# Kernel tuning notes

Hardware: AMD Instinct MI355X
Metric: run time of the kernel (lower is better)

## Reference

```python
import jax, jax.numpy as jnp
import numpy as np
from jax import lax

B, DIM, H, W = 8, 256, 48, 48
HEADS, DH = 8, 32
K, S = 5, 2
P = K // 2
SCALE = DH ** -0.5
EPS = 1e-5


def setup_inputs() -> dict:
    key = jax.random.key(0)
    ks = jax.random.split(key, 12)
    w = lambda k, sh: jax.random.normal(k, sh, jnp.float32) * 0.02
    return {
        'x': jax.random.normal(ks[0], (B, DIM, H, W), jnp.float32),
        'kv': jax.random.normal(ks[1], (B, DIM, H, W), jnp.float32),
        'wq': w(ks[2], (DIM, DIM)), 'bq': jnp.zeros((DIM,), jnp.float32),
        'wk': w(ks[3], (DIM, DIM)), 'bk': jnp.zeros((DIM,), jnp.float32),
        'wv': w(ks[4], (DIM, DIM)), 'bv': jnp.zeros((DIM,), jnp.float32),
        'w_dw': w(ks[5], (DH, 1, K, K)), 'b_dw': jnp.zeros((DH,), jnp.float32),
        'ln_w': jnp.ones((DH,), jnp.float32), 'ln_b': jnp.zeros((DH,), jnp.float32),
        'w_off': w(ks[6], (2, DH)),
        'wo': w(ks[7], (DIM, DIM)), 'bo': jnp.zeros((DIM,), jnp.float32),
    }


def conv1x1(x, w, b=None):
    # x: (B, Cin, H, W), w: (Cout, Cin)
    y = jnp.einsum('oc,bchw->bohw', w, x)
    return y if b is None else y + b[None, :, None, None]


def grid_sample_bilinear(inp, grid):
    # inp: (N, C, Hh, Ww); grid: (N, Hg, Wg, 2) in (x, y), align_corners=True
    N, C, Hh, Ww = inp.shape
    gx = (grid[..., 0] + 1.0) * 0.5 * (Ww - 1)
    gy = (grid[..., 1] + 1.0) * 0.5 * (Hh - 1)
    x0 = jnp.floor(gx)
    y0 = jnp.floor(gy)
    wx = gx - x0  # frac weights for x1/y1 corners
    wy = gy - y0
    x0i = jnp.clip(x0.astype(jnp.int32), 0, Ww - 1)
    x1i = jnp.clip(x0.astype(jnp.int32) + 1, 0, Ww - 1)
    y0i = jnp.clip(y0.astype(jnp.int32), 0, Hh - 1)
    y1i = jnp.clip(y0.astype(jnp.int32) + 1, 0, Hh - 1)
    flat = inp.reshape(N, C, Hh * Ww)
    n = grid.shape[1] * grid.shape[2]

    def gather(yi, xi):
        idx = (yi * Ww + xi).reshape(N, 1, n)
        return jnp.take_along_axis(flat, jnp.broadcast_to(idx, (N, C, n)), axis=2)

    w00 = ((1 - wx) * (1 - wy)).reshape(N, 1, n)
    w01 = (wx * (1 - wy)).reshape(N, 1, n)
    w10 = ((1 - wx) * wy).reshape(N, 1, n)
    w11 = (wx * wy).reshape(N, 1, n)
    return (w00 * gather(y0i, x0i) + w01 * gather(y0i, x1i)
            + w10 * gather(y1i, x0i) + w11 * gather(y1i, x1i))  # (N, C, n)


def reference(x, kv, wq, bq, wk, bk, wv, bv, w_dw, b_dw, ln_w, ln_b, w_off, wo, bo):
    q = conv1x1(x, wq, bq)                      # (B, DIM, H, W)
    q_off = q.reshape(B * HEADS, DH, H, W)      # per-head channels
    # depthwise offset conv
    t = lax.conv_general_dilated(q_off, w_dw, (S, S), [(P, P), (P, P)],
                                 feature_group_count=DH,
                                 dimension_numbers=('NCHW', 'OIHW', 'NCHW'))
    t = t + b_dw[None, :, None, None]
    Hk, Wk = t.shape[2], t.shape[3]
    n = Hk * Wk
    # LayerNormProxy: LN over channel dim
    t = t.transpose(0, 2, 3, 1)                 # (BH, Hk, Wk, DH)
    mu = t.mean(-1, keepdims=True)
    var = ((t - mu) ** 2).mean(-1, keepdims=True)
    t = (t - mu) / jnp.sqrt(var + EPS) * ln_w + ln_b
    t = jax.nn.gelu(t, approximate=False)
    offset = jnp.einsum('oc,bhwc->bhwo', w_off, t)  # (BH, Hk, Wk, 2) as (y, x)
    # reference points, normalized to [-1, 1]
    ref_y = (jnp.linspace(0.5, Hk - 0.5, Hk, dtype=jnp.float32) / (Hk - 1.0)) * 2.0 - 1.0
    ref_x = (jnp.linspace(0.5, Wk - 0.5, Wk, dtype=jnp.float32) / (Wk - 1.0)) * 2.0 - 1.0
    ref = jnp.stack(jnp.meshgrid(ref_y, ref_x, indexing='ij'), axis=-1)  # (Hk, Wk, 2)
    pos = jnp.clip(offset + ref[None], -1.0, 1.0)
    grid = pos[..., ::-1]                       # (x, y) order for sampling
    kvs = grid_sample_bilinear(kv.reshape(B * HEADS, DH, H, W), grid)  # (BH, DH, n)
    kv4 = kvs.reshape(B, DIM, 1, n)
    k = conv1x1(kv4, wk, bk).reshape(B * HEADS, DH, n)
    v = conv1x1(kv4, wv, bv).reshape(B * HEADS, DH, n)
    qf = q.reshape(B * HEADS, DH, H * W)
    attn = jax.nn.softmax(jnp.einsum('bcm,bcn->bmn', qf, k) * SCALE, axis=2)
    out = jnp.einsum('bmn,bcn->bcm', attn, v).reshape(B, DIM, H, W)
    return conv1x1(out, wo, bo)
```

## Files before the change

### kernel.cpp

```cpp
#include <hip/hip_runtime.h>
#include <hip/hip_bf16.h>
#include <cstddef>

#define BB 8
#define DIM 256
#define HH 48
#define WW 48
#define HW 2304
#define HEADS 8
#define DH 32
#define BH 64
#define HK 24
#define WK 24
#define NN 576
#define SCALE 0.17677669529663687f
#define EPSF 1e-5f

typedef __attribute__((ext_vector_type(8))) short short8;
typedef __attribute__((ext_vector_type(4))) float f32x4;

static __device__ inline short f2bf_s(float f) {
  __hip_bfloat16 h = __float2bfloat16(f);
  return *reinterpret_cast<short*>(&h);
}

static __device__ inline unsigned pkrnd(float a, float b) {
  unsigned ua = __builtin_bit_cast(unsigned, a) + 0x8000u;
  unsigned ub = __builtin_bit_cast(unsigned, b) + 0x8000u;
  return __builtin_amdgcn_perm(ub, ua, 0x07060302);
}

static __device__ inline void split8(const float* xf, short8& bh, short8& bl) {
  union { unsigned u[4]; short8 v; } H, L;
#pragma unroll
  for (int p = 0; p < 4; p++) {
    float x0 = xf[2 * p], x1 = xf[2 * p + 1];
    unsigned u0 = __builtin_bit_cast(unsigned, x0) & 0xffff0000u;
    unsigned u1 = __builtin_bit_cast(unsigned, x1) & 0xffff0000u;
    float l0 = x0 - __builtin_bit_cast(float, u0);
    float l1 = x1 - __builtin_bit_cast(float, u1);
    H.u[p] = __builtin_amdgcn_perm(u1, u0, 0x07060302);
    L.u[p] = __builtin_amdgcn_perm(__builtin_bit_cast(unsigned, l1),
                                   __builtin_bit_cast(unsigned, l0), 0x07060302);
  }
  bh = H.v;
  bl = L.v;
}

__global__ __launch_bounds__(256) void prep(
    const float* __restrict__ x, const float* __restrict__ kv,
    const float* __restrict__ wq, const float* __restrict__ wk,
    const float* __restrict__ wv, const float* __restrict__ wo,
    short* __restrict__ Xh, short* __restrict__ Xl,
    float* __restrict__ kvT,
    short* __restrict__ Wqh, short* __restrict__ Wql,
    short* __restrict__ Wkh, short* __restrict__ Wkl,
    short* __restrict__ Wvh, short* __restrict__ Wvl,
    short* __restrict__ Woh, short* __restrict__ Wol) {
  __shared__ float t[64][65];
  const int bid = blockIdx.x;
  if (bid < 1152) {
    int mt = bid % 36, t2 = bid / 36;
    int ct = t2 & 3, b = t2 >> 2;
    const int c0 = ct * 64, m0 = mt * 64;
    const int col = threadIdx.x & 63, row4 = threadIdx.x >> 6;
    const float* xb = x + ((size_t)b * 256 + c0) * HW + m0;
#pragma unroll
    for (int k = 0; k < 16; k++) {
      int c = row4 + k * 4;
      t[c][col] = xb[(size_t)c * HW + col];
    }
    __syncthreads();
    short* oh = Xh + ((size_t)b * HW + m0) * 256 + c0;
    short* ol = Xl + ((size_t)b * HW + m0) * 256 + c0;
#pragma unroll
    for (int k = 0; k < 16; k++) {
      int m = row4 + k * 4;
      float v = t[col][m];
      unsigned u = __builtin_bit_cast(unsigned, v) & 0xffff0000u;
      float rem = v - __builtin_bit_cast(float, u);
      oh[(size_t)m * 256 + col] = (short)(u >> 16);
      ol[(size_t)m * 256 + col] = (short)(__builtin_bit_cast(unsigned, rem) >> 16);
    }
  } else if (bid < 2304) {
    int bb = bid - 1152;
    int mt = bb % 36, t2 = bb / 36;
    int ct = t2 & 3, b = t2 >> 2;
    const int c0 = ct * 64, m0 = mt * 64;
    const int col = threadIdx.x & 63, row4 = threadIdx.x >> 6;
    const float* xb = kv + ((size_t)b * 256 + c0) * HW + m0;
#pragma unroll
    for (int k = 0; k < 16; k++) {
      int c = row4 + k * 4;
      t[c][col] = xb[(size_t)c * HW + col];
    }
    __syncthreads();
    float* ot = kvT + ((size_t)b * HW + m0) * 256 + c0;
#pragma unroll
    for (int k = 0; k < 16; k++) {
      int m = row4 + k * 4;
      ot[(size_t)m * 256 + col] = t[col][m];
    }
  } else {
    const float* srcs[4] = {wq, wk, wv, wo};
    short* his[4] = {Wqh, Wkh, Wvh, Woh};
    short* los[4] = {Wql, Wkl, Wvl, Wol};
    int e0 = (bid - 2304) * 1024 + threadIdx.x * 4;
    int w = e0 >> 16, off = e0 & 65535;
    float4 v4 = *(const float4*)(srcs[w] + off);
    float vv[4] = {v4.x, v4.y, v4.z, v4.w};
    union { short s[4]; int2 i2; } Hu, Lu;
#pragma unroll
    for (int j = 0; j < 4; j++) {
      unsigned u = __builtin_bit_cast(unsigned, vv[j]) & 0xffff0000u;
      float rem = vv[j] - __builtin_bit_cast(float, u);
      Hu.s[j] = (short)(u >> 16);
      Lu.s[j] = (short)(__builtin_bit_cast(unsigned, rem) >> 16);
    }
    *(int2*)(his[w] + off) = Hu.i2;
    *(int2*)(los[w] + off) = Lu.i2;
  }
}

__global__ __launch_bounds__(256) void gemm_q_mfma(const short* __restrict__ Wh,
                                                   const short* __restrict__ Wl,
                                                   const float* __restrict__ bias,
                                                   const short* __restrict__ Xh,
                                                   const short* __restrict__ Xl,
                                                   float* __restrict__ Y) {
  const int tid = threadIdx.x;
  const int wave = tid >> 6;
  const int lane = tid & 63;
  const int quad = lane >> 4, l15 = lane & 15;
  const int b = blockIdx.y;
  const int oBase = wave * 64;
  const int mBase = blockIdx.x * 64;

  f32x4 acc[4][4] = {};
  for (int kc = 0; kc < 256; kc += 32) {
    short8 ah[4], al[4];
#pragma unroll
    for (int os = 0; os < 4; os++) {
      ah[os] = *(const short8*)(Wh + (size_t)(oBase + os * 16 + l15) * 256 + kc + quad * 8);
      al[os] = *(const short8*)(Wl + (size_t)(oBase + os * 16 + l15) * 256 + kc + quad * 8);
    }
#pragma unroll
    for (int mt = 0; mt < 4; mt++) {
      short8 bh_ = *(const short8*)(Xh + ((size_t)b * HW + mBase + mt * 16 + l15) * 256 + kc + quad * 8);
      short8 bl_ = *(const short8*)(Xl + ((size_t)b * HW + mBase + mt * 16 + l15) * 256 + kc + quad * 8);
#pragma unroll
      for (int os = 0; os < 4; os++) {
        acc[os][mt] = __builtin_amdgcn_mfma_f32_16x16x32_bf16(ah[os], bh_, acc[os][mt], 0, 0, 0);
        acc[os][mt] = __builtin_amdgcn_mfma_f32_16x16x32_bf16(al[os], bh_, acc[os][mt], 0, 0, 0);
        acc[os][mt] = __builtin_amdgcn_mfma_f32_16x16x32_bf16(ah[os], bl_, acc[os][mt], 0, 0, 0);
      }
    }
  }

#pragma unroll
  for (int os = 0; os < 4; os++)
#pragma unroll
    for (int r = 0; r < 4; r++) {
      int o = oBase + os * 16 + quad * 4 + r;
      float bs = bias[o];
      float* yp = Y + ((size_t)b * 256 + o) * HW + mBase + l15;
#pragma unroll
      for (int mt = 0; mt < 4; mt++) yp[mt * 16] = acc[os][mt][r] + bs;
    }
}

#define QPS 101
__global__ __launch_bounds__(256) void dw_sample_kernel(
    const float* __restrict__ q, const float* __restrict__ kvT,
    const float* __restrict__ w_dw, const float* __restrict__ b_dw,
    const float* __restrict__ ln_w, const float* __restrict__ ln_b,
    const float* __restrict__ w_off, short* __restrict__ kvsTh,
    short* __restrict__ kvsTl) {
  __shared__ float s_q[32 * QPS];
  __shared__ float s_w[DH * 25];
  const int tid = threadIdx.x;
  const int ch = tid & 31;
  const int np = tid >> 5;
  const int bid = blockIdx.x;
  const int b = bid & 7;
  const int r = bid >> 3;
  const int head = r / 72;
  const int rr = r - head * 72;
  const int yk = rr / 3;
  const int xk0 = (rr - yk * 3) * 8;
  const int bh = b * 8 + head;
  const int xk = xk0 + np;
  const int n = yk * WK + xk;

  for (int i = tid; i < DH * 25; i += 256) s_w[i] = w_dw[i];

  {
    const int y0 = yk * 2 - 2, x0 = xk0 * 2 - 2;
    const float* qbh = q + (size_t)bh * DH * HW;
#pragma unroll
    for (int it = 0; it < 13; it++) {
      int e = it * 256 + tid;
      if (e < 3200) {
        int c = e / 100;
        int rem = e - c * 100;
        int dy = rem / 20;
        int xl = rem - dy * 20;
        int gy = y0 + dy, gx = x0 + xl;
        float v = 0.f;
        if ((unsigned)gy < HH && (unsigned)gx < WW)
          v = qbh[(size_t)c * HW + gy * WW + gx];
        s_q[c * QPS + dy * 20 + xl] = v;
      }
    }
  }
  __syncthreads();

  float t = b_dw[ch];
  {
    const float* wp = s_w + ch * 25;
    const float* qp = s_q + ch * QPS + np * 2;
#pragma unroll
    for (int dy = 0; dy < 5; dy++)
#pragma unroll
      for (int dx = 0; dx < 5; dx++)
        t += wp[dy * 5 + dx] * qp[dy * 20 + dx];
  }

  float mu = t;
#pragma unroll
  for (int m = 1; m < 32; m <<= 1) mu += __shfl_xor(mu, m);
  mu *= (1.0f / DH);
  float d = t - mu;
  float var = d * d;
#pragma unroll
  for (int m = 1; m < 32; m <<= 1) var += __shfl_xor(var, m);
  var *= (1.0f / DH);
  float rstd = rsqrtf(var + EPSF);

  float xn = d * rstd * ln_w[ch] + ln_b[ch];
  float g = 0.5f * xn * (1.0f + erff(xn * 0.70710678118654752f));
  float o0 = w_off[ch] * g;
  float o1 = w_off[DH + ch] * g;
#pragma unroll
  for (int m = 1; m < 32; m <<= 1) {
    o0 += __shfl_xor(o0, m);
    o1 += __shfl_xor(o1, m);
  }

  const float ref_y = (0.5f + (float)yk) / 23.0f * 2.0f - 1.0f;
  const float ref_x = (0.5f + (float)xk) / 23.0f * 2.0f - 1.0f;
  float py = fminf(fmaxf(o0 + ref_y, -1.0f), 1.0f);
  float px = fminf(fmaxf(o1 + ref_x, -1.0f), 1.0f);

  float gx = (px + 1.0f) * 0.5f * 47.0f;
  float gy = (py + 1.0f) * 0.5f * 47.0f;
  float x0f = floorf(gx), y0f = floorf(gy);
  float wx = gx - x0f, wy = gy - y0f;
  int x0 = (int)x0f, y0 = (int)y0f;
  int x0i = min(max(x0, 0), WW - 1);
  int x1i = min(max(x0 + 1, 0), WW - 1);
  int y0i = min(max(y0, 0), HH - 1);
  int y1i = min(max(y0 + 1, 0), HH - 1);
  float w00 = (1.f - wx) * (1.f - wy);
  float w01 = wx * (1.f - wy);
  float w10 = (1.f - wx) * wy;
  float w11 = wx * wy;

  const float* kvb = kvT + (size_t)b * HW * 256 + head * DH + ch;
  float val = w00 * kvb[(size_t)(y0i * WW + x0i) * 256]
            + w01 * kvb[(size_t)(y0i * WW + x1i) * 256]
            + w10 * kvb[(size_t)(y1i * WW + x0i) * 256]
            + w11 * kvb[(size_t)(y1i * WW + x1i) * 256];

  unsigned ub = __builtin_bit_cast(unsigned, val);
  unsigned uh = ub & 0xffff0000u;
  float rem = val - __builtin_bit_cast(float, uh);
  size_t idx = ((size_t)b * NN + n) * 256 + head * DH + ch;
  kvsTh[idx] = (short)(uh >> 16);
  kvsTl[idx] = (short)(__builtin_bit_cast(unsigned, rem) >> 16);
}

__global__ __launch_bounds__(256) void kv_gemm_mfma(
    const short* __restrict__ Wkh, const short* __restrict__ Wkl,
    const float* __restrict__ bk,
    const short* __restrict__ Wvh, const short* __restrict__ Wvl,
    const float* __restrict__ bv,
    const short* __restrict__ Xh, const short* __restrict__ Xl,
    short* __restrict__ Kb, short* __restrict__ Vb) {
  const int tid = threadIdx.x;
  const int wave = tid >> 6;
  const int lane = tid & 63;
  const int quad = lane >> 4, l15 = lane & 15;
  const int b = blockIdx.z;
  const int mode = blockIdx.y >> 2;
  const int oTile = (blockIdx.y & 3) * 64;
  const int nBase = blockIdx.x * 64;

  if (mode == 0) {
    const int nW = nBase + wave * 16;
    const short* arh = Xh + ((size_t)b * NN + nW + l15) * 256 + quad * 8;
    const short* arl = Xl + ((size_t)b * NN + nW + l15) * 256 + quad * 8;
    f32x4 acc[4] = {};
    for (int kc = 0; kc < 256; kc += 32) {
      short8 ah = *(const short8*)(arh + kc);
      short8 al = *(const short8*)(arl + kc);
#pragma unroll
      for (int ot = 0; ot < 4; ot++) {
        short8 bh_ = *(const short8*)(Wkh + (size_t)(oTile + ot * 16 + l15) * 256 + kc + quad * 8);
        short8 bl_ = *(const short8*)(Wkl + (size_t)(oTile + ot * 16 + l15) * 256 + kc + quad * 8);
        acc[ot] = __builtin_amdgcn_mfma_f32_16x16x32_bf16(ah, bh_, acc[ot], 0, 0, 0);
        acc[ot] = __builtin_amdgcn_mfma_f32_16x16x32_bf16(al, bh_, acc[ot], 0, 0, 0);
        acc[ot] = __builtin_amdgcn_mfma_f32_16x16x32_bf16(ah, bl_, acc[ot], 0, 0, 0);
      }
    }
    float bs[4];
#pragma unroll
    for (int ot = 0; ot < 4; ot++) bs[ot] = bk[oTile + ot * 16 + l15];
#pragma unroll
    for (int r = 0; r < 4; r++) {
      short* yp = Kb + ((size_t)b * NN + nW + quad * 4 + r) * 256 + oTile + l15;
#pragma unroll
      for (int ot = 0; ot < 4; ot++) yp[ot * 16] = f2bf_s(acc[ot][r] + bs[ot]);
    }
  } else {
    const int oW = oTile + wave * 16;
    const short* arh = Wvh + (size_t)(oW + l15) * 256 + quad * 8;
    const short* arl = Wvl + (size_t)(oW + l15) * 256 + quad * 8;
    f32x4 acc[4] = {};
    for (int kc = 0; kc < 256; kc += 32) {
      short8 ah = *(const short8*)(arh + kc);
      short8 al = *(const short8*)(arl + kc);
#pragma unroll
      for (int nt = 0; nt < 4; nt++) {
        short8 bh_ = *(const short8*)(Xh + ((size_t)b * NN + nBase + nt * 16 + l15) * 256 + kc + quad * 8);
        short8 bl_ = *(const short8*)(Xl + ((size_t)b * NN + nBase + nt * 16 + l15) * 256 + kc + quad * 8);
        acc[nt] = __builtin_amdgcn_mfma_f32_16x16x32_bf16(ah, bh_, acc[nt], 0, 0, 0);
        acc[nt] = __builtin_amdgcn_mfma_f32_16x16x32_bf16(al, bh_, acc[nt], 0, 0, 0);
        acc[nt] = __builtin_amdgcn_mfma_f32_16x16x32_bf16(ah, bl_, acc[nt], 0, 0, 0);
      }
    }
#pragma unroll
    for (int r = 0; r < 4; r++) {
      int o = oW + quad * 4 + r;
      float bs = bv[o];
      short* yp = Vb + ((size_t)b * 256 + o) * NN + nBase + l15;
#pragma unroll
      for (int nt = 0; nt < 4; nt++) yp[nt * 16] = f2bf_s(acc[nt][r] + bs);
    }
  }
}

__global__ __launch_bounds__(256) void attn_mfma(const float* __restrict__ q,
                                                 const short* __restrict__ Kb,
                                                 const short* __restrict__ Vb,
                                                 short* __restrict__ O) {
  __shared__ short sK[2][64 * 40];
  __shared__ short sV[2][32 * 88];
  __shared__ int sP[4][2][256];
  const int tid = threadIdx.x;
  const int wave = tid >> 6;
  const int lane = tid & 63;
  const int quad = lane >> 4;
  const int l15 = lane & 15;
  const int bh = blockIdx.y;
  const int b = bh >> 3, head = bh & 7;
  const int mBase = blockIdx.x * 128 + wave * 32;

  short8 bq[2];
#pragma unroll
  for (int mt = 0; mt < 2; mt++) {
    const float* qp = q + ((size_t)bh * DH + quad * 8) * HW + mBase + mt * 16 + l15;
    short8 v;
#pragma unroll
    for (int j = 0; j < 8; j++) v[j] = f2bf_s(qp[(size_t)j * HW] * SCALE);
    bq[mt] = v;
  }

  const int kn = tid >> 2, kc = (tid & 3) * 8;
  const int vc = tid >> 3, vn = (tid & 7) * 8;
  const short* kg = Kb + (size_t)b * NN * 256 + head * DH;
  const short* vg = Vb + ((size_t)b * 256 + head * DH) * NN;

  short8 kreg = *(const short8*)(kg + (size_t)kn * 256 + kc);
  short8 vreg = *(const short8*)(vg + (size_t)vc * NN + vn);
  *(short8*)(&sK[0][kn * 40 + kc]) = kreg;
  *(short8*)(&sV[0][vc * 88 + vn]) = vreg;
  __syncthreads();

  const int g = (l15 >> 1) & 3;
  const int row16 = l15 * 16;
  const int wr0 = row16 + (((quad >> 1) ^ g) << 2) + ((quad & 1) << 1);
  const int wr1 = row16 + (((2 + (quad >> 1)) ^ g) << 2) + ((quad & 1) << 1);
  const int rd = row16 + ((quad ^ g) << 2);

  f32x4 oacc[2][2] = {};
  f32x4 dacc[2] = {};
  const short ONE = 0x3F80;
  const short8 ones = {ONE, ONE, ONE, ONE, ONE, ONE, ONE, ONE};

  for (int s = 0; s < 9; s++) {
    const int buf = s & 1;
    if (s + 1 < 9) {
      kreg = *(const short8*)(kg + (size_t)((s + 1) * 64 + kn) * 256 + kc);
      vreg = *(const short8*)(vg + (size_t)vc * NN + (s + 1) * 64 + vn);
    }
#pragma unroll
    for (int nt = 0; nt < 2; nt++) {
      short8 ka0 = *(const short8*)(&sK[buf][(nt * 32 + l15) * 40 + quad * 8]);
      short8 ka1 = *(const short8*)(&sK[buf][(nt * 32 + 16 + l15) * 40 + quad * 8]);
      short8 va0 = *(const short8*)(&sV[buf][l15 * 88 + nt * 32 + quad * 8]);
      short8 va1 = *(const short8*)(&sV[buf][(16 + l15) * 88 + nt * 32 + quad * 8]);
      f32x4 z = {0.f, 0.f, 0.f, 0.f};
      f32x4 st[2][2];
      st[0][0] = __builtin_amdgcn_mfma_f32_16x16x32_bf16(ka0, bq[0], z, 0, 0, 0);
      st[0][1] = __builtin_amdgcn_mfma_f32_16x16x32_bf16(ka1, bq[0], z, 0, 0, 0);
      st[1][0] = __builtin_amdgcn_mfma_f32_16x16x32_bf16(ka0, bq[1], z, 0, 0, 0);
      st[1][1] = __builtin_amdgcn_mfma_f32_16x16x32_bf16(ka1, bq[1], z, 0, 0, 0);
#pragma unroll
      for (int mt = 0; mt < 2; mt++) {
        float p0 = __expf(st[mt][0][0]), p1 = __expf(st[mt][0][1]);
        float p2 = __expf(st[mt][0][2]), p3 = __expf(st[mt][0][3]);
        float p4 = __expf(st[mt][1][0]), p5 = __expf(st[mt][1][1]);
        float p6 = __expf(st[mt][1][2]), p7 = __expf(st[mt][1][3]);
        int* base = &sP[wave][mt][0];
        *(int2*)(base + wr0) = make_int2((int)pkrnd(p0, p1), (int)pkrnd(p2, p3));
        *(int2*)(base + wr1) = make_int2((int)pkrnd(p4, p5), (int)pkrnd(p6, p7));
      }
#pragma unroll
      for (int mt = 0; mt < 2; mt++) {
        short8 pa = *(short8*)(&sP[wave][mt][0] + rd);
        oacc[mt][0] = __builtin_amdgcn_mfma_f32_16x16x32_bf16(pa, va0, oacc[mt][0], 0, 0, 0);
        oacc[mt][1] = __builtin_amdgcn_mfma_f32_16x16x32_bf16(pa, va1, oacc[mt][1], 0, 0, 0);
        dacc[mt] = __builtin_amdgcn_mfma_f32_16x16x32_bf16(pa, ones, dacc[mt], 0, 0, 0);
      }
    }
    if (s + 1 < 9) {
      *(short8*)(&sK[buf ^ 1][kn * 40 + kc]) = kreg;
      *(short8*)(&sV[buf ^ 1][vc * 88 + vn]) = vreg;
    }
    __syncthreads();
  }

#pragma unroll
  for (int mt = 0; mt < 2; mt++) {
    short* ob = O + ((size_t)b * HW + mBase + mt * 16) * 256 + head * DH + l15;
#pragma unroll
    for (int r = 0; r < 4; r++) {
      float inv = 1.0f / dacc[mt][r];
      ob[(size_t)(quad * 4 + r) * 256] = f2bf_s(oacc[mt][0][r] * inv);
      ob[(size_t)(quad * 4 + r) * 256 + 16] = f2bf_s(oacc[mt][1][r] * inv);
    }
  }
}

__global__ __launch_bounds__(256) void wo_gemm_mfma(const short* __restrict__ Whi,
                                                    const short* __restrict__ Wlo,
                                                    const float* __restrict__ bias,
                                                    const short* __restrict__ X,
                                                    float* __restrict__ Y) {
  const int tid = threadIdx.x;
  const int wave = tid >> 6;
  const int lane = tid & 63;
  const int quad = lane >> 4;
  const int l15 = lane & 15;
  const int b = blockIdx.y;
  const int oBase = wave * 64;
  const int mBase = blockIdx.x * 64;

  f32x4 acc[4][4] = {};
  for (int kc = 0; kc < 256; kc += 32) {
    short8 ah[4], al[4];
#pragma unroll
    for (int os = 0; os < 4; os++) {
      ah[os] = *(const short8*)(Whi + (size_t)(oBase + os * 16 + l15) * 256 + kc + quad * 8);
      al[os] = *(const short8*)(Wlo + (size_t)(oBase + os * 16 + l15) * 256 + kc + quad * 8);
    }
#pragma unroll
    for (int mt = 0; mt < 4; mt++) {
      short8 bx = *(const short8*)(X + ((size_t)b * HW + mBase + mt * 16 + l15) * 256 + kc + quad * 8);
#pragma unroll
      for (int os = 0; os < 4; os++) {
        acc[os][mt] = __builtin_amdgcn_mfma_f32_16x16x32_bf16(ah[os], bx, acc[os][mt], 0, 0, 0);
        acc[os][mt] = __builtin_amdgcn_mfma_f32_16x16x32_bf16(al[os], bx, acc[os][mt], 0, 0, 0);
      }
    }
  }

#pragma unroll
  for (int os = 0; os < 4; os++)
#pragma unroll
    for (int r = 0; r < 4; r++) {
      int o = oBase + os * 16 + quad * 4 + r;
      float bs = bias[o];
      float* yp = Y + ((size_t)b * 256 + o) * HW + mBase + l15;
#pragma unroll
      for (int mt = 0; mt < 4; mt++) yp[mt * 16] = acc[os][mt][r] + bs;
    }
}

extern "C" void kernel_launch(void* const* d_in, const int* in_sizes, int n_in,
                              void* d_out, int out_size, void* d_ws, size_t ws_size,
                              hipStream_t stream) {
  const float* x    = (const float*)d_in[0];
  const float* kv   = (const float*)d_in[1];
  const float* wq   = (const float*)d_in[2];
  const float* bq   = (const float*)d_in[3];
  const float* wk   = (const float*)d_in[4];
  const float* bk   = (const float*)d_in[5];
  const float* wv   = (const float*)d_in[6];
  const float* bv   = (const float*)d_in[7];
  const float* w_dw = (const float*)d_in[8];
  const float* b_dw = (const float*)d_in[9];
  const float* ln_w = (const float*)d_in[10];
  const float* ln_b = (const float*)d_in[11];
  const float* w_off= (const float*)d_in[12];
  const float* wo   = (const float*)d_in[13];
  const float* bo   = (const float*)d_in[14];
  float* out = (float*)d_out;
  float* ws = (float*)d_ws;

  float* q     = ws;
  short* Xth   = (short*)(ws + 4718592);
  short* O     = (short*)(ws + 4718592);
  short* Xtl   = (short*)(ws + 7077888);
  short* kvsTh = (short*)(ws + 7077888);
  short* kvsTl = (short*)(ws + 7667712);
  short* Kb    = (short*)(ws + 8257536);
  short* Vb    = (short*)(ws + 8847360);
  short* Wqh   = (short*)(ws + 9437184);
  short* Wql = Wqh + 65536;
  short* Wkh = Wql + 65536;
  short* Wkl = Wkh + 65536;
  short* Wvh = Wkl + 65536;
  short* Wvl = Wvh + 65536;
  short* Woh = Wvl + 65536;
  short* Wol = Woh + 65536;
  float* kvT = out;

  prep<<<dim3(2560), dim3(256), 0, stream>>>(x, kv, wq, wk, wv, wo, Xth, Xtl, kvT,
                                             Wqh, Wql, Wkh, Wkl, Wvh, Wvl, Woh, Wol);
  gemm_q_mfma<<<dim3(HW / 64, BB), dim3(256), 0, stream>>>(Wqh, Wql, bq, Xth, Xtl, q);
  dw_sample_kernel<<<dim3(BH * NN / 8), dim3(256), 0, stream>>>(
      q, kvT, w_dw, b_dw, ln_w, ln_b, w_off, kvsTh, kvsTl);
  kv_gemm_mfma<<<dim3(NN / 64, 8, BB), dim3(256), 0, stream>>>(
      Wkh, Wkl, bk, Wvh, Wvl, bv, kvsTh, kvsTl, Kb, Vb);
  attn_mfma<<<dim3(HW / 128, BH), dim3(256), 0, stream>>>(q, Kb, Vb, O);
  wo_gemm_mfma<<<dim3(HW / 64, BB), dim3(256), 0, stream>>>(Woh, Wol, bo, O, out);
}
```

Before: 254.5 us.

## Co-schedule kv transpose and weight splits with Q GEMM; stage activations in LDS

Moves the kv transpose and the wk/wv/wo hi/lo split out of the prep kernel and into the Q-projection GEMM launch as extra block ranges, so that independent work overlaps with the GEMM. The Q and Wo GEMMs now use 512-thread blocks that stage the 64-row activation tile into XOR-swizzled shared memory and split the output channels across 8 waves instead of 4. The aim is to cut redundant global loads of the activation tile and raise parallelism per block. In exchange, each block uses 64KB of LDS in the fused GEMM, which may limit occupancy.

```diff
diff --git a/kernel.cpp b/kernel.cpp
--- a/kernel.cpp
+++ b/kernel.cpp
@@ -30,33 +30,10 @@
   return __builtin_amdgcn_perm(ub, ua, 0x07060302);
 }
 
-static __device__ inline void split8(const float* xf, short8& bh, short8& bl) {
-  union { unsigned u[4]; short8 v; } H, L;
-#pragma unroll
-  for (int p = 0; p < 4; p++) {
-    float x0 = xf[2 * p], x1 = xf[2 * p + 1];
-    unsigned u0 = __builtin_bit_cast(unsigned, x0) & 0xffff0000u;
-    unsigned u1 = __builtin_bit_cast(unsigned, x1) & 0xffff0000u;
-    float l0 = x0 - __builtin_bit_cast(float, u0);
-    float l1 = x1 - __builtin_bit_cast(float, u1);
-    H.u[p] = __builtin_amdgcn_perm(u1, u0, 0x07060302);
-    L.u[p] = __builtin_amdgcn_perm(__builtin_bit_cast(unsigned, l1),
-                                   __builtin_bit_cast(unsigned, l0), 0x07060302);
-  }
-  bh = H.v;
-  bl = L.v;
-}
-
 __global__ __launch_bounds__(256) void prep(
-    const float* __restrict__ x, const float* __restrict__ kv,
-    const float* __restrict__ wq, const float* __restrict__ wk,
-    const float* __restrict__ wv, const float* __restrict__ wo,
+    const float* __restrict__ x, const float* __restrict__ wq,
     short* __restrict__ Xh, short* __restrict__ Xl,
-    float* __restrict__ kvT,
-    short* __restrict__ Wqh, short* __restrict__ Wql,
-    short* __restrict__ Wkh, short* __restrict__ Wkl,
-    short* __restrict__ Wvh, short* __restrict__ Wvl,
-    short* __restrict__ Woh, short* __restrict__ Wol) {
+    short* __restrict__ Wqh, short* __restrict__ Wql) {
   __shared__ float t[64][65];
   const int bid = blockIdx.x;
   if (bid < 1152) {
@@ -82,32 +59,9 @@
       oh[(size_t)m * 256 + col] = (short)(u >> 16);
       ol[(size_t)m * 256 + col] = (short)(__builtin_bit_cast(unsigned, rem) >> 16);
     }
-  } else if (bid < 2304) {
-    int bb = bid - 1152;
-    int mt = bb % 36, t2 = bb / 36;
-    int ct = t2 & 3, b = t2 >> 2;
-    const int c0 = ct * 64, m0 = mt * 64;
-    const int col = threadIdx.x & 63, row4 = threadIdx.x >> 6;
-    const float* xb = kv + ((size_t)b * 256 + c0) * HW + m0;
-#pragma unroll
-    for (int k = 0; k < 16; k++) {
-      int c = row4 + k * 4;
-      t[c][col] = xb[(size_t)c * HW + col];
-    }
-    __syncthreads();
-    float* ot = kvT + ((size_t)b * HW + m0) * 256 + c0;
-#pragma unroll
-    for (int k = 0; k < 16; k++) {
-      int m = row4 + k * 4;
-      ot[(size_t)m * 256 + col] = t[col][m];
-    }
   } else {
-    const float* srcs[4] = {wq, wk, wv, wo};
-    short* his[4] = {Wqh, Wkh, Wvh, Woh};
-    short* los[4] = {Wql, Wkl, Wvl, Wol};
-    int e0 = (bid - 2304) * 1024 + threadIdx.x * 4;
-    int w = e0 >> 16, off = e0 & 65535;
-    float4 v4 = *(const float4*)(srcs[w] + off);
+    int e0 = (bid - 1152) * 1024 + threadIdx.x * 4;
+    float4 v4 = *(const float4*)(wq + e0);
     float vv[4] = {v4.x, v4.y, v4.z, v4.w};
     union { short s[4]; int2 i2; } Hu, Lu;
 #pragma unroll
@@ -117,56 +71,116 @@
       Hu.s[j] = (short)(u >> 16);
       Lu.s[j] = (short)(__builtin_bit_cast(unsigned, rem) >> 16);
     }
+    *(int2*)(Wqh + e0) = Hu.i2;
+    *(int2*)(Wql + e0) = Lu.i2;
+  }
+}
+
+__global__ __launch_bounds__(512) void gemm_q_fused(
+    const short* __restrict__ Wh, const short* __restrict__ Wl,
+    const float* __restrict__ bias,
+    const short* __restrict__ Xh, const short* __restrict__ Xl,
+    float* __restrict__ Y,
+    const float* __restrict__ kv, float* __restrict__ kvT,
+    const float* __restrict__ wk, const float* __restrict__ wv,
+    const float* __restrict__ wo,
+    short* __restrict__ Wkh, short* __restrict__ Wkl,
+    short* __restrict__ Wvh, short* __restrict__ Wvl,
+    short* __restrict__ Woh, short* __restrict__ Wol) {
+  __shared__ short sB[2][64 * 256];
+  const int bid = blockIdx.x;
+  const int tid = threadIdx.x;
+
+  if (bid < 288) {
+    const int b = bid / 36;
+    const int mBase = (bid % 36) * 64;
+    const short* srcH = Xh + ((size_t)b * HW + mBase) * 256;
+    const short* srcL = Xl + ((size_t)b * HW + mBase) * 256;
+#pragma unroll
+    for (int it = 0; it < 4; it++) {
+      int idx = it * 512 + tid;
+      int row = idx >> 5, ck = idx & 31;
+      int dst = row * 256 + ((ck ^ (row & 7)) << 3);
+      *(short8*)(&sB[0][dst]) = *(const short8*)(srcH + (size_t)row * 256 + ck * 8);
+      *(short8*)(&sB[1][dst]) = *(const short8*)(srcL + (size_t)row * 256 + ck * 8);
+    }
+    __syncthreads();
+
+    const int wave = tid >> 6, lane = tid & 63;
+    const int quad = lane >> 4, l15 = lane & 15;
+    const int oBase = wave * 32;
+    f32x4 acc[2][4] = {};
+    for (int kc = 0; kc < 256; kc += 32) {
+      short8 ah[2], al[2];
+#pragma unroll
+      for (int os = 0; os < 2; os++) {
+        ah[os] = *(const short8*)(Wh + (size_t)(oBase + os * 16 + l15) * 256 + kc + quad * 8);
+        al[os] = *(const short8*)(Wl + (size_t)(oBase + os * 16 + l15) * 256 + kc + quad * 8);
+      }
+#pragma unroll
+      for (int mt = 0; mt < 4; mt++) {
+        int row = mt * 16 + l15;
+        int off = row * 256 + ((((kc >> 3) + quad) ^ (row & 7)) << 3);
+        short8 bh_ = *(const short8*)(&sB[0][off]);
+        short8 bl_ = *(const short8*)(&sB[1][off]);
+#pragma unroll
+        for (int os = 0; os < 2; os++) {
+          acc[os][mt] = __builtin_amdgcn_mfma_f32_16x16x32_bf16(ah[os], bh_, acc[os][mt], 0, 0, 0);
+          acc[os][mt] = __builtin_amdgcn_mfma_f32_16x16x32_bf16(al[os], bh_, acc[os][mt], 0, 0, 0);
+          acc[os][mt] = __builtin_amdgcn_mfma_f32_16x16x32_bf16(ah[os], bl_, acc[os][mt], 0, 0, 0);
+        }
+      }
+    }
+#pragma unroll
+    for (int os = 0; os < 2; os++)
+#pragma unroll
+      for (int r = 0; r < 4; r++) {
+        int o = oBase + os * 16 + quad * 4 + r;
+        float bs = bias[o];
+        float* yp = Y + ((size_t)b * 256 + o) * HW + mBase + l15;
+#pragma unroll
+        for (int mt = 0; mt < 4; mt++) yp[mt * 16] = acc[os][mt][r] + bs;
+      }
+  } else if (bid < 1440) {
+    float* tf = (float*)sB;
+    int bb = bid - 288;
+    int mt = bb % 36, t2 = bb / 36;
+    int ct = t2 & 3, b = t2 >> 2;
+    const int c0 = ct * 64, m0 = mt * 64;
+    const int col = tid & 63, row8 = tid >> 6;
+    const float* xb = kv + ((size_t)b * 256 + c0) * HW + m0;
+#pragma unroll
+    for (int k = 0; k < 8; k++) {
+      int c = row8 + k * 8;
+      tf[c * 65 + col] = xb[(size_t)c * HW + col];
+    }
+    __syncthreads();
+    float* ot = kvT + ((size_t)b * HW + m0) * 256 + c0;
+#pragma unroll
+    for (int k = 0; k < 8; k++) {
+      int m = row8 + k * 8;
+      ot[(size_t)m * 256 + col] = tf[col * 65 + m];
+    }
+  } else {
+    const float* srcs[3] = {wk, wv, wo};
+    short* his[3] = {Wkh, Wvh, Woh};
+    short* los[3] = {Wkl, Wvl, Wol};
+    int bb = bid - 1440;
+    int w = bb >> 5;
+    int off = (bb & 31) * 2048 + tid * 4;
+    float4 v4 = *(const float4*)(srcs[w] + off);
+    float vv[4] = {v4.x, v4.y, v4.z, v4.w};
+    union { short s[4]; int2 i2; } Hu, Lu;
+#pragma unroll
+    for (int j = 0; j < 4; j++) {
+      unsigned u = __builtin_bit_cast(unsigned, vv[j]) & 0xffff0000u;
+      float rem = vv[j] - __builtin_bit_cast(float, u);
+      Hu.s[j] = (short)(u >> 16);
+      Lu.s[j] = (short)(__builtin_bit_cast(unsigned, rem) >> 16);
+    }
     *(int2*)(his[w] + off) = Hu.i2;
     *(int2*)(los[w] + off) = Lu.i2;
   }
-}
-
-__global__ __launch_bounds__(256) void gemm_q_mfma(const short* __restrict__ Wh,
-                                                   const short* __restrict__ Wl,
-                                                   const float* __restrict__ bias,
-                                                   const short* __restrict__ Xh,
-                                                   const short* __restrict__ Xl,
-                                                   float* __restrict__ Y) {
-  const int tid = threadIdx.x;
-  const int wave = tid >> 6;
-  const int lane = tid & 63;
-  const int quad = lane >> 4, l15 = lane & 15;
-  const int b = blockIdx.y;
-  const int oBase = wave * 64;
-  const int mBase = blockIdx.x * 64;
-
-  f32x4 acc[4][4] = {};
-  for (int kc = 0; kc < 256; kc += 32) {
-    short8 ah[4], al[4];
-#pragma unroll
-    for (int os = 0; os < 4; os++) {
-      ah[os] = *(const short8*)(Wh + (size_t)(oBase + os * 16 + l15) * 256 + kc + quad * 8);
-      al[os] = *(const short8*)(Wl + (size_t)(oBase + os * 16 + l15) * 256 + kc + quad * 8);
-    }
-#pragma unroll
-    for (int mt = 0; mt < 4; mt++) {
-      short8 bh_ = *(const short8*)(Xh + ((size_t)b * HW + mBase + mt * 16 + l15) * 256 + kc + quad * 8);
-      short8 bl_ = *(const short8*)(Xl + ((size_t)b * HW + mBase + mt * 16 + l15) * 256 + kc + quad * 8);
-#pragma unroll
-      for (int os = 0; os < 4; os++) {
-        acc[os][mt] = __builtin_amdgcn_mfma_f32_16x16x32_bf16(ah[os], bh_, acc[os][mt], 0, 0, 0);
-        acc[os][mt] = __builtin_amdgcn_mfma_f32_16x16x32_bf16(al[os], bh_, acc[os][mt], 0, 0, 0);
-        acc[os][mt] = __builtin_amdgcn_mfma_f32_16x16x32_bf16(ah[os], bl_, acc[os][mt], 0, 0, 0);
-      }
-    }
-  }
-
-#pragma unroll
-  for (int os = 0; os < 4; os++)
-#pragma unroll
-    for (int r = 0; r < 4; r++) {
-      int o = oBase + os * 16 + quad * 4 + r;
-      float bs = bias[o];
-      float* yp = Y + ((size_t)b * 256 + o) * HW + mBase + l15;
-#pragma unroll
-      for (int mt = 0; mt < 4; mt++) yp[mt * 16] = acc[os][mt][r] + bs;
-    }
 }
 
 #define QPS 101
@@ -453,33 +467,44 @@
   }
 }
 
-__global__ __launch_bounds__(256) void wo_gemm_mfma(const short* __restrict__ Whi,
+__global__ __launch_bounds__(512) void wo_gemm_mfma(const short* __restrict__ Whi,
                                                     const short* __restrict__ Wlo,
                                                     const float* __restrict__ bias,
                                                     const short* __restrict__ X,
                                                     float* __restrict__ Y) {
+  __shared__ short sX[64 * 256];
   const int tid = threadIdx.x;
-  const int wave = tid >> 6;
-  const int lane = tid & 63;
-  const int quad = lane >> 4;
-  const int l15 = lane & 15;
   const int b = blockIdx.y;
-  const int oBase = wave * 64;
   const int mBase = blockIdx.x * 64;
 
-  f32x4 acc[4][4] = {};
+  const short* src = X + ((size_t)b * HW + mBase) * 256;
+#pragma unroll
+  for (int it = 0; it < 4; it++) {
+    int idx = it * 512 + tid;
+    int row = idx >> 5, ck = idx & 31;
+    *(short8*)(&sX[row * 256 + ((ck ^ (row & 7)) << 3)]) =
+        *(const short8*)(src + (size_t)row * 256 + ck * 8);
+  }
+  __syncthreads();
+
+  const int wave = tid >> 6, lane = tid & 63;
+  const int quad = lane >> 4, l15 = lane & 15;
+  const int oBase = wave * 32;
+
+  f32x4 acc[2][4] = {};
   for (int kc = 0; kc < 256; kc += 32) {
-    short8 ah[4], al[4];
-#pragma unroll
-    for (int os = 0; os < 4; os++) {
+    short8 ah[2], al[2];
+#pragma unroll
+    for (int os = 0; os < 2; os++) {
       ah[os] = *(const short8*)(Whi + (size_t)(oBase + os * 16 + l15) * 256 + kc + quad * 8);
       al[os] = *(const short8*)(Wlo + (size_t)(oBase + os * 16 + l15) * 256 + kc + quad * 8);
     }
 #pragma unroll
     for (int mt = 0; mt < 4; mt++) {
-      short8 bx = *(const short8*)(X + ((size_t)b * HW + mBase + mt * 16 + l15) * 256 + kc + quad * 8);
-#pragma unroll
-      for (int os = 0; os < 4; os++) {
+      int row = mt * 16 + l15;
+      short8 bx = *(const short8*)(&sX[row * 256 + ((((kc >> 3) + quad) ^ (row & 7)) << 3)]);
+#pragma unroll
+      for (int os = 0; os < 2; os++) {
         acc[os][mt] = __builtin_amdgcn_mfma_f32_16x16x32_bf16(ah[os], bx, acc[os][mt], 0, 0, 0);
         acc[os][mt] = __builtin_amdgcn_mfma_f32_16x16x32_bf16(al[os], bx, acc[os][mt], 0, 0, 0);
       }
@@ -487,7 +512,7 @@
   }
 
 #pragma unroll
-  for (int os = 0; os < 4; os++)
+  for (int os = 0; os < 2; os++)
 #pragma unroll
     for (int r = 0; r < 4; r++) {
       int o = oBase + os * 16 + quad * 4 + r;
@@ -537,13 +562,14 @@
   short* Wol = Woh + 65536;
   float* kvT = out;
 
-  prep<<<dim3(2560), dim3(256), 0, stream>>>(x, kv, wq, wk, wv, wo, Xth, Xtl, kvT,
-                                             Wqh, Wql, Wkh, Wkl, Wvh, Wvl, Woh, Wol);
-  gemm_q_mfma<<<dim3(HW / 64, BB), dim3(256), 0, stream>>>(Wqh, Wql, bq, Xth, Xtl, q);
+  prep<<<dim3(1216), dim3(256), 0, stream>>>(x, wq, Xth, Xtl, Wqh, Wql);
+  gemm_q_fused<<<dim3(1536), dim3(512), 0, stream>>>(
+      Wqh, Wql, bq, Xth, Xtl, q,
+      kv, kvT, wk, wv, wo, Wkh, Wkl, Wvh, Wvl, Woh, Wol);
   dw_sample_kernel<<<dim3(BH * NN / 8), dim3(256), 0, stream>>>(
       q, kvT, w_dw, b_dw, ln_w, ln_b, w_off, kvsTh, kvsTl);
   kv_gemm_mfma<<<dim3(NN / 64, 8, BB), dim3(256), 0, stream>>>(
       Wkh, Wkl, bk, Wvh, Wvl, bv, kvsTh, kvsTl, Kb, Vb);
   attn_mfma<<<dim3(HW / 128, BH), dim3(256), 0, stream>>>(q, Kb, Vb, O);
-  wo_gemm_mfma<<<dim3(HW / 64, BB), dim3(256), 0, stream>>>(Woh, Wol, bo, O, out);
-}
+  wo_gemm_mfma<<<dim3(HW / 64, BB), dim3(512), 0, stream>>>(Woh, Wol, bo, O, out);
+}
```

After: 230.7 us. 1.1x faster.
